# Performance work log

Hardware: AMD Instinct MI355X
Metric: run time of the kernel (lower is better)

Reference implementation:

```python
import jax, jax.numpy as jnp
import numpy as np

TEMPERATURE = 0.07
EPS = 1e-8  # torch cosine_similarity norm clamp


def setup_inputs() -> dict:
    key = jax.random.key(0)
    k1, k2 = jax.random.split(key)
    B, d = 8192, 256
    X = jax.random.normal(k1, (B, d), dtype=jnp.float32)
    Y = jax.random.normal(k2, (B, d), dtype=jnp.float32)
    return {"X": X, "Y": Y}


def _normalize(v):
    # torch cosine_similarity clamps the norm at eps
    n = jnp.sqrt(jnp.sum(v * v, axis=-1, keepdims=True))
    return v / jnp.maximum(n, EPS)


def reference(X, Y):
    # cosine similarity matrix via normalize + GEMM (same math as broadcasted
    # cosine_similarity(X.unsqueeze(1), Y.unsqueeze(0), dim=-1))
    Xn = _normalize(X)                      # [B, d]
    Yn = _normalize(Y)                      # [B, d]
    logits = (Xn @ Yn.T) / TEMPERATURE      # [B, B]
    # cross_entropy with targets = arange(B): mean of -log_softmax diagonal
    logp = jax.nn.log_softmax(logits, axis=-1)
    loss = -jnp.mean(jnp.diagonal(logp))
    return loss
```

## Files before the change

kernel.cpp:

```cpp
#include <hip/hip_runtime.h>
#include <hip/hip_bf16.h>


typedef __attribute__((ext_vector_type(2)))  float f32x2;
typedef __attribute__((ext_vector_type(4)))  float f32x4;
typedef __attribute__((ext_vector_type(4)))  int   i32x4;
typedef __attribute__((ext_vector_type(8)))  int   i32x8;

#define AS1(p) ((const __attribute__((address_space(1))) void*)(uintptr_t)(p))
#define AS3(p) ((__attribute__((address_space(3))) void*)(uintptr_t)(p))

constexpr int   BROWS = 8192;
constexpr int   DDIM  = 256;
constexpr float kInvT = 14.285714285714286f;
constexpr float kC1   = 20.609929155556622f;
constexpr float kLn2  = 0.6931471805599453f;
constexpr int   kSC   = 0x7F7F7F7F;

#if __has_builtin(__builtin_amdgcn_exp2f)
#define EXP2F(x) __builtin_amdgcn_exp2f(x)
#else
#define EXP2F(x) exp2f(x)
#endif
#if __has_builtin(__builtin_amdgcn_logf)
#define LOG2F(x) __builtin_amdgcn_logf(x)
#else
#define LOG2F(x) log2f(x)
#endif

static __device__ __forceinline__ unsigned f2fp8(float f) {
  unsigned u = __builtin_bit_cast(unsigned, f);
  unsigned s = (u >> 24) & 0x80u;
  float af = __builtin_fabsf(f);
  if (af < 0.015625f) {
    int q = (int)__builtin_rintf(af * 512.0f);
    return s | (unsigned)q;
  }
  unsigned au = u & 0x7FFFFFFFu;
  au += 0x7FFFFu + ((au >> 20) & 1u);
  unsigned e8 = ((au >> 23) - 127u + 7u) & 0xFu;
  unsigned m  = (au >> 20) & 7u;
  return s | (e8 << 3) | m;
}

__global__ __launch_bounds__(256) void nrm_kernel(
    const float* __restrict__ X, const float* __restrict__ Y,
    unsigned int* __restrict__ Xq, unsigned int* __restrict__ Yq,
    float* __restrict__ diag, float* __restrict__ row_sum)
{
  const int wave = threadIdx.x >> 6;
  const int lane = threadIdx.x & 63;
  const int row  = blockIdx.x * 4 + wave;
  const float4 x = *(const float4*)(X + (size_t)row * DDIM + lane * 4);
  const float4 y = *(const float4*)(Y + (size_t)row * DDIM + lane * 4);
  float ssx = x.x*x.x + x.y*x.y + x.z*x.z + x.w*x.w;
  float ssy = y.x*y.x + y.y*y.y + y.z*y.z + y.w*y.w;
  float dot = x.x*y.x + x.y*y.y + x.z*y.z + x.w*y.w;
  #pragma unroll
  for (int m = 1; m < 64; m <<= 1) {
    ssx += __shfl_xor(ssx, m);
    ssy += __shfl_xor(ssy, m);
    dot += __shfl_xor(dot, m);
  }
  const float invx = 1.0f / fmaxf(sqrtf(ssx), 1e-8f);
  const float invy = 1.0f / fmaxf(sqrtf(ssy), 1e-8f);
#if __has_builtin(__builtin_amdgcn_cvt_pk_fp8_f32)
  int xq = __builtin_amdgcn_cvt_pk_fp8_f32(x.x * invx, x.y * invx, 0, false);
  xq     = __builtin_amdgcn_cvt_pk_fp8_f32(x.z * invx, x.w * invx, xq, true);
  int yq = __builtin_amdgcn_cvt_pk_fp8_f32(y.x * invy, y.y * invy, 0, false);
  yq     = __builtin_amdgcn_cvt_pk_fp8_f32(y.z * invy, y.w * invy, yq, true);
#else
  int xq = (int)(f2fp8(x.x*invx) | (f2fp8(x.y*invx) << 8) |
                 (f2fp8(x.z*invx) << 16) | (f2fp8(x.w*invx) << 24));
  int yq = (int)(f2fp8(y.x*invy) | (f2fp8(y.y*invy) << 8) |
                 (f2fp8(y.z*invy) << 16) | (f2fp8(y.w*invy) << 24));
#endif
  Xq[row * 64 + lane] = (unsigned)xq;
  Yq[row * 64 + lane] = (unsigned)yq;
  if (lane == 0) {
    diag[row] = dot * invx * invy * kInvT;
    row_sum[row] = 0.0f;
  }
}

static __device__ __forceinline__ void expq(const f32x4& pv, f32x2 (&sm)[2]) {
  f32x2 v0 = { pv[0], pv[1] };
  f32x2 v1 = { pv[2], pv[3] };
  v0 = v0 * kC1 + (f32x2){-kC1, -kC1};
  v1 = v1 * kC1 + (f32x2){-kC1, -kC1};
  sm[0] += (f32x2){ EXP2F(v0.x), EXP2F(v0.y) };
  sm[1] += (f32x2){ EXP2F(v1.x), EXP2F(v1.y) };
}

static __device__ __forceinline__ void tile_step(
    const char* __restrict__ tb, const int (&bb)[2], const i32x8 (&a)[4][2],
    f32x4 (&cur)[4][2], f32x4 (&prev)[4][2], f32x2 (&sums2)[4][2])
{
  const f32x4 cz = {0.f, 0.f, 0.f, 0.f};
  {
    const i32x4 lo0 = *(const i32x4*)(tb + (bb[0]));
    const i32x4 hi0 = *(const i32x4*)(tb + (bb[0] ^ 16));
    const i32x4 lo1 = *(const i32x4*)(tb + (bb[1]));
    const i32x4 hi1 = *(const i32x4*)(tb + (bb[1] ^ 16));
    const i32x8 b0 = __builtin_shufflevector(lo0, hi0, 0, 1, 2, 3, 4, 5, 6, 7);
    const i32x8 b1 = __builtin_shufflevector(lo1, hi1, 0, 1, 2, 3, 4, 5, 6, 7);
    cur[0][0] = __builtin_amdgcn_mfma_scale_f32_16x16x128_f8f6f4(a[0][0], b0, cz, 0, 0, 0, kSC, 0, kSC);
    cur[0][1] = __builtin_amdgcn_mfma_scale_f32_16x16x128_f8f6f4(a[0][0], b1, cz, 0, 0, 0, kSC, 0, kSC);
    expq(prev[0][0], sums2[0]);
    cur[1][0] = __builtin_amdgcn_mfma_scale_f32_16x16x128_f8f6f4(a[1][0], b0, cz, 0, 0, 0, kSC, 0, kSC);
    cur[1][1] = __builtin_amdgcn_mfma_scale_f32_16x16x128_f8f6f4(a[1][0], b1, cz, 0, 0, 0, kSC, 0, kSC);
    expq(prev[1][0], sums2[1]);
    cur[2][0] = __builtin_amdgcn_mfma_scale_f32_16x16x128_f8f6f4(a[2][0], b0, cz, 0, 0, 0, kSC, 0, kSC);
    cur[2][1] = __builtin_amdgcn_mfma_scale_f32_16x16x128_f8f6f4(a[2][0], b1, cz, 0, 0, 0, kSC, 0, kSC);
    expq(prev[2][0], sums2[2]);
    cur[3][0] = __builtin_amdgcn_mfma_scale_f32_16x16x128_f8f6f4(a[3][0], b0, cz, 0, 0, 0, kSC, 0, kSC);
    cur[3][1] = __builtin_amdgcn_mfma_scale_f32_16x16x128_f8f6f4(a[3][0], b1, cz, 0, 0, 0, kSC, 0, kSC);
    expq(prev[3][0], sums2[3]);
  }
  {
    const i32x4 lo0 = *(const i32x4*)(tb + (bb[0] ^ 128));
    const i32x4 hi0 = *(const i32x4*)(tb + (bb[0] ^ 144));
    const i32x4 lo1 = *(const i32x4*)(tb + (bb[1] ^ 128));
    const i32x4 hi1 = *(const i32x4*)(tb + (bb[1] ^ 144));
    const i32x8 b0 = __builtin_shufflevector(lo0, hi0, 0, 1, 2, 3, 4, 5, 6, 7);
    const i32x8 b1 = __builtin_shufflevector(lo1, hi1, 0, 1, 2, 3, 4, 5, 6, 7);
    cur[0][0] = __builtin_amdgcn_mfma_scale_f32_16x16x128_f8f6f4(a[0][1], b0, cur[0][0], 0, 0, 0, kSC, 0, kSC);
    cur[0][1] = __builtin_amdgcn_mfma_scale_f32_16x16x128_f8f6f4(a[0][1], b1, cur[0][1], 0, 0, 0, kSC, 0, kSC);
    expq(prev[0][1], sums2[0]);
    cur[1][0] = __builtin_amdgcn_mfma_scale_f32_16x16x128_f8f6f4(a[1][1], b0, cur[1][0], 0, 0, 0, kSC, 0, kSC);
    cur[1][1] = __builtin_amdgcn_mfma_scale_f32_16x16x128_f8f6f4(a[1][1], b1, cur[1][1], 0, 0, 0, kSC, 0, kSC);
    expq(prev[1][1], sums2[1]);
    cur[2][0] = __builtin_amdgcn_mfma_scale_f32_16x16x128_f8f6f4(a[2][1], b0, cur[2][0], 0, 0, 0, kSC, 0, kSC);
    cur[2][1] = __builtin_amdgcn_mfma_scale_f32_16x16x128_f8f6f4(a[2][1], b1, cur[2][1], 0, 0, 0, kSC, 0, kSC);
    expq(prev[2][1], sums2[2]);
    cur[3][0] = __builtin_amdgcn_mfma_scale_f32_16x16x128_f8f6f4(a[3][1], b0, cur[3][0], 0, 0, 0, kSC, 0, kSC);
    cur[3][1] = __builtin_amdgcn_mfma_scale_f32_16x16x128_f8f6f4(a[3][1], b1, cur[3][1], 0, 0, 0, kSC, 0, kSC);
    expq(prev[3][1], sums2[3]);
  }
}

__global__ __launch_bounds__(256, 2) void logits_kernel(
    const unsigned char* __restrict__ Xq,
    const unsigned char* __restrict__ Yq,
    float* __restrict__ row_sum)
{
  __shared__ char lds[4 * 8192];
  const int tid  = threadIdx.x;
  const int lane = tid & 63;
  const int wave = tid >> 6;
  const int l15  = lane & 15;
  const int g    = lane >> 4;

  const int bid  = blockIdx.x;
  const int xcd  = bid & 7;
  const int idx  = bid >> 3;
  const int panel = (xcd >> 2) * 16 + (idx & 15);
  const int split = (xcd & 3) * 4 + (idx >> 4);

  const int rowbase = panel * 256 + wave * 64;
  const char* Xb = (const char*)Xq;
  const char* Yb = (const char*)Yq + (size_t)split * (512 * 256);

  i32x8 a[4][2];
  #pragma unroll
  for (int m = 0; m < 4; ++m) {
    const char* rp = Xb + (size_t)(rowbase + m * 16 + l15) * 256 + g * 32;
    a[m][0] = *(const i32x8*)(rp);
    a[m][1] = *(const i32x8*)(rp + 128);
  }

  f32x2 sums2[4][2];
  #pragma unroll
  for (int m = 0; m < 4; ++m) {
    sums2[m][0] = (f32x2){0.f, 0.f};
    sums2[m][1] = (f32x2){0.f, 0.f};
  }

  int bb[2];
  #pragma unroll
  for (int n = 0; n < 2; ++n)
    bb[n] = (n * 16 + l15) * 256 + (((2 * g) ^ l15) << 4);

  auto stage = [&](int t, int buf) {
    const char* Yt = Yb + (size_t)t * 8192;
    char* db = lds + buf * 8192;
    #pragma unroll
    for (int s = 0; s < 2; ++s) {
      const int portion = (s * 4 + wave) * 1024;
      const int L = portion + lane * 16;
      const int src = (L & ~255) | ((L & 255) ^ (((L >> 8) & 15) << 4));
      __builtin_amdgcn_global_load_lds(AS1(Yt + src), AS3(db + portion), 16, 0, 0);
    }
  };

  f32x4 accA[4][2], accB[4][2];
  #pragma unroll
  for (int m = 0; m < 4; ++m)
    #pragma unroll
    for (int n = 0; n < 2; ++n) {
      accA[m][n] = (f32x4){0.f, 0.f, 0.f, 0.f};
      const float ni = -__builtin_inff();
      accB[m][n] = (f32x4){ni, ni, ni, ni};
    }

  stage(0, 0);
  stage(1, 1);
  stage(2, 2);
  #pragma unroll 1
  for (int p = 0; p < 8; ++p) {
    const int t = 2 * p;
    if (p < 7) asm volatile("s_waitcnt vmcnt(4)" ::: "memory");
    else       asm volatile("s_waitcnt vmcnt(2)" ::: "memory");
    __builtin_amdgcn_s_barrier();
    if (t + 3 < 16) stage(t + 3, (t + 3) & 3);
    tile_step(lds + (t & 3) * 8192, bb, a, accA, accB, sums2);
    if (p < 7) asm volatile("s_waitcnt vmcnt(4)" ::: "memory");
    else       asm volatile("s_waitcnt vmcnt(0)" ::: "memory");
    __builtin_amdgcn_s_barrier();
    if (t + 4 < 16) stage(t + 4, (t + 4) & 3);
    tile_step(lds + ((t + 1) & 3) * 8192, bb, a, accB, accA, sums2);
  }
  #pragma unroll
  for (int m = 0; m < 4; ++m) {
    expq(accB[m][0], sums2[m]);
    expq(accB[m][1], sums2[m]);
  }

  #pragma unroll
  for (int m = 0; m < 4; ++m)
    #pragma unroll
    for (int h = 0; h < 2; ++h)
      #pragma unroll
      for (int r2 = 0; r2 < 2; ++r2) {
        float s = (r2 == 0) ? sums2[m][h].x : sums2[m][h].y;
        s += __shfl_xor(s, 1);
        s += __shfl_xor(s, 2);
        s += __shfl_xor(s, 4);
        s += __shfl_xor(s, 8);
        if (l15 == 0)
          atomicAdd(row_sum + rowbase + m * 16 + g * 4 + h * 2 + r2, s);
      }
}

__global__ __launch_bounds__(1024) void loss_kernel(
    const float* __restrict__ row_sum, const float* __restrict__ diag,
    float* __restrict__ out)
{
  const int t = threadIdx.x;
  double acc = 0.0;
  #pragma unroll
  for (int h = 0; h < 2; ++h) {
    const int i = h * 4096 + t * 4;
    const float4 s = *(const float4*)(row_sum + i);
    const float4 d = *(const float4*)(diag + i);
    acc += (double)(kInvT + LOG2F(s.x) * kLn2 - d.x);
    acc += (double)(kInvT + LOG2F(s.y) * kLn2 - d.y);
    acc += (double)(kInvT + LOG2F(s.z) * kLn2 - d.z);
    acc += (double)(kInvT + LOG2F(s.w) * kLn2 - d.w);
  }
  #pragma unroll
  for (int m = 1; m < 64; m <<= 1) acc += __shfl_xor(acc, m);
  __shared__ double red[16];
  if ((t & 63) == 0) red[t >> 6] = acc;
  __syncthreads();
  if (t == 0) {
    double tot = 0.0;
    #pragma unroll
    for (int w = 0; w < 16; ++w) tot += red[w];
    out[0] = (float)(tot / (double)BROWS);
  }
}

extern "C" void kernel_launch(void* const* d_in, const int* in_sizes, int n_in,
                              void* d_out, int out_size, void* d_ws, size_t ws_size,
                              hipStream_t stream) {
  (void)in_sizes; (void)n_in; (void)out_size; (void)ws_size;
  const float* X = (const float*)d_in[0];
  const float* Y = (const float*)d_in[1];
  char* w = (char*)d_ws;
  unsigned int* Xq = (unsigned int*)(w);
  unsigned int* Yq = (unsigned int*)(w + (2u << 20));
  float* diag    = (float*)(w + (4u << 20));
  float* row_sum = (float*)(w + (4u << 20) + (32u << 10));

  nrm_kernel<<<BROWS / 4, 256, 0, stream>>>(X, Y, Xq, Yq, diag, row_sum);
  logits_kernel<<<512, 256, 0, stream>>>((const unsigned char*)Xq,
                                         (const unsigned char*)Yq, row_sum);
  loss_kernel<<<1, 1024, 0, stream>>>(row_sum, diag, (float*)d_out);
}
```

Before: 35.43 us.

## Prefetch next tile's first-K B fragments from LDS into registers

Each tile step now loads the first-half B fragments of the following LDS tile into registers while it runs MFMAs on the current tile. The current tile's first-half fragments come from the previous step, and a prologue loads the first tile's fragments. The goal is to hide LDS read latency in front of the first MFMA group. In exchange, the global-to-LDS waits are tightened from vmcnt(4) to vmcnt(2) so the next tile is resident one step earlier, which leaves less slack for global load latency and adds register pressure.

Result: no change. 35.14 us (-0.8%).

```diff
diff --git a/kernel.cpp b/kernel.cpp
--- a/kernel.cpp
+++ b/kernel.cpp
@@ -27,6 +27,9 @@
 #else
 #define LOG2F(x) log2f(x)
 #endif
+
+#define MFMA __builtin_amdgcn_mfma_scale_f32_16x16x128_f8f6f4
+#define SHUF(lo, hi) __builtin_shufflevector(lo, hi, 0, 1, 2, 3, 4, 5, 6, 7)
 
 static __device__ __forceinline__ unsigned f2fp8(float f) {
   unsigned u = __builtin_bit_cast(unsigned, f);
@@ -92,51 +95,51 @@
   sm[1] += (f32x2){ EXP2F(v1.x), EXP2F(v1.y) };
 }
 
-static __device__ __forceinline__ void tile_step(
-    const char* __restrict__ tb, const int (&bb)[2], const i32x8 (&a)[4][2],
+static __device__ __forceinline__ void tile_compute(
+    const char* __restrict__ tb_cur, const char* __restrict__ tb_next,
+    bool doNext, const int (&bb)[2], const i32x8 (&a)[4][2],
+    i32x8 (&bK0)[2], i32x8 (&bN)[2],
     f32x4 (&cur)[4][2], f32x4 (&prev)[4][2], f32x2 (&sums2)[4][2])
 {
   const f32x4 cz = {0.f, 0.f, 0.f, 0.f};
-  {
-    const i32x4 lo0 = *(const i32x4*)(tb + (bb[0]));
-    const i32x4 hi0 = *(const i32x4*)(tb + (bb[0] ^ 16));
-    const i32x4 lo1 = *(const i32x4*)(tb + (bb[1]));
-    const i32x4 hi1 = *(const i32x4*)(tb + (bb[1] ^ 16));
-    const i32x8 b0 = __builtin_shufflevector(lo0, hi0, 0, 1, 2, 3, 4, 5, 6, 7);
-    const i32x8 b1 = __builtin_shufflevector(lo1, hi1, 0, 1, 2, 3, 4, 5, 6, 7);
-    cur[0][0] = __builtin_amdgcn_mfma_scale_f32_16x16x128_f8f6f4(a[0][0], b0, cz, 0, 0, 0, kSC, 0, kSC);
-    cur[0][1] = __builtin_amdgcn_mfma_scale_f32_16x16x128_f8f6f4(a[0][0], b1, cz, 0, 0, 0, kSC, 0, kSC);
-    expq(prev[0][0], sums2[0]);
-    cur[1][0] = __builtin_amdgcn_mfma_scale_f32_16x16x128_f8f6f4(a[1][0], b0, cz, 0, 0, 0, kSC, 0, kSC);
-    cur[1][1] = __builtin_amdgcn_mfma_scale_f32_16x16x128_f8f6f4(a[1][0], b1, cz, 0, 0, 0, kSC, 0, kSC);
-    expq(prev[1][0], sums2[1]);
-    cur[2][0] = __builtin_amdgcn_mfma_scale_f32_16x16x128_f8f6f4(a[2][0], b0, cz, 0, 0, 0, kSC, 0, kSC);
-    cur[2][1] = __builtin_amdgcn_mfma_scale_f32_16x16x128_f8f6f4(a[2][0], b1, cz, 0, 0, 0, kSC, 0, kSC);
-    expq(prev[2][0], sums2[2]);
-    cur[3][0] = __builtin_amdgcn_mfma_scale_f32_16x16x128_f8f6f4(a[3][0], b0, cz, 0, 0, 0, kSC, 0, kSC);
-    cur[3][1] = __builtin_amdgcn_mfma_scale_f32_16x16x128_f8f6f4(a[3][0], b1, cz, 0, 0, 0, kSC, 0, kSC);
-    expq(prev[3][0], sums2[3]);
-  }
-  {
-    const i32x4 lo0 = *(const i32x4*)(tb + (bb[0] ^ 128));
-    const i32x4 hi0 = *(const i32x4*)(tb + (bb[0] ^ 144));
-    const i32x4 lo1 = *(const i32x4*)(tb + (bb[1] ^ 128));
-    const i32x4 hi1 = *(const i32x4*)(tb + (bb[1] ^ 144));
-    const i32x8 b0 = __builtin_shufflevector(lo0, hi0, 0, 1, 2, 3, 4, 5, 6, 7);
-    const i32x8 b1 = __builtin_shufflevector(lo1, hi1, 0, 1, 2, 3, 4, 5, 6, 7);
-    cur[0][0] = __builtin_amdgcn_mfma_scale_f32_16x16x128_f8f6f4(a[0][1], b0, cur[0][0], 0, 0, 0, kSC, 0, kSC);
-    cur[0][1] = __builtin_amdgcn_mfma_scale_f32_16x16x128_f8f6f4(a[0][1], b1, cur[0][1], 0, 0, 0, kSC, 0, kSC);
-    expq(prev[0][1], sums2[0]);
-    cur[1][0] = __builtin_amdgcn_mfma_scale_f32_16x16x128_f8f6f4(a[1][1], b0, cur[1][0], 0, 0, 0, kSC, 0, kSC);
-    cur[1][1] = __builtin_amdgcn_mfma_scale_f32_16x16x128_f8f6f4(a[1][1], b1, cur[1][1], 0, 0, 0, kSC, 0, kSC);
-    expq(prev[1][1], sums2[1]);
-    cur[2][0] = __builtin_amdgcn_mfma_scale_f32_16x16x128_f8f6f4(a[2][1], b0, cur[2][0], 0, 0, 0, kSC, 0, kSC);
-    cur[2][1] = __builtin_amdgcn_mfma_scale_f32_16x16x128_f8f6f4(a[2][1], b1, cur[2][1], 0, 0, 0, kSC, 0, kSC);
-    expq(prev[2][1], sums2[2]);
-    cur[3][0] = __builtin_amdgcn_mfma_scale_f32_16x16x128_f8f6f4(a[3][1], b0, cur[3][0], 0, 0, 0, kSC, 0, kSC);
-    cur[3][1] = __builtin_amdgcn_mfma_scale_f32_16x16x128_f8f6f4(a[3][1], b1, cur[3][1], 0, 0, 0, kSC, 0, kSC);
-    expq(prev[3][1], sums2[3]);
-  }
+  const i32x4 lo0 = *(const i32x4*)(tb_cur + (bb[0] ^ 128));
+  const i32x4 hi0 = *(const i32x4*)(tb_cur + (bb[0] ^ 144));
+  const i32x4 lo1 = *(const i32x4*)(tb_cur + (bb[1] ^ 128));
+  const i32x4 hi1 = *(const i32x4*)(tb_cur + (bb[1] ^ 144));
+  if (doNext) {
+    const i32x4 nlo0 = *(const i32x4*)(tb_next + bb[0]);
+    const i32x4 nhi0 = *(const i32x4*)(tb_next + (bb[0] ^ 16));
+    const i32x4 nlo1 = *(const i32x4*)(tb_next + bb[1]);
+    const i32x4 nhi1 = *(const i32x4*)(tb_next + (bb[1] ^ 16));
+    bN[0] = SHUF(nlo0, nhi0);
+    bN[1] = SHUF(nlo1, nhi1);
+  }
+  cur[0][0] = MFMA(a[0][0], bK0[0], cz, 0, 0, 0, kSC, 0, kSC);
+  cur[0][1] = MFMA(a[0][0], bK0[1], cz, 0, 0, 0, kSC, 0, kSC);
+  expq(prev[0][0], sums2[0]);
+  cur[1][0] = MFMA(a[1][0], bK0[0], cz, 0, 0, 0, kSC, 0, kSC);
+  cur[1][1] = MFMA(a[1][0], bK0[1], cz, 0, 0, 0, kSC, 0, kSC);
+  expq(prev[1][0], sums2[1]);
+  cur[2][0] = MFMA(a[2][0], bK0[0], cz, 0, 0, 0, kSC, 0, kSC);
+  cur[2][1] = MFMA(a[2][0], bK0[1], cz, 0, 0, 0, kSC, 0, kSC);
+  expq(prev[2][0], sums2[2]);
+  cur[3][0] = MFMA(a[3][0], bK0[0], cz, 0, 0, 0, kSC, 0, kSC);
+  cur[3][1] = MFMA(a[3][0], bK0[1], cz, 0, 0, 0, kSC, 0, kSC);
+  expq(prev[3][0], sums2[3]);
+  const i32x8 b10 = SHUF(lo0, hi0);
+  const i32x8 b11 = SHUF(lo1, hi1);
+  cur[0][0] = MFMA(a[0][1], b10, cur[0][0], 0, 0, 0, kSC, 0, kSC);
+  cur[0][1] = MFMA(a[0][1], b11, cur[0][1], 0, 0, 0, kSC, 0, kSC);
+  expq(prev[0][1], sums2[0]);
+  cur[1][0] = MFMA(a[1][1], b10, cur[1][0], 0, 0, 0, kSC, 0, kSC);
+  cur[1][1] = MFMA(a[1][1], b11, cur[1][1], 0, 0, 0, kSC, 0, kSC);
+  expq(prev[1][1], sums2[1]);
+  cur[2][0] = MFMA(a[2][1], b10, cur[2][0], 0, 0, 0, kSC, 0, kSC);
+  cur[2][1] = MFMA(a[2][1], b11, cur[2][1], 0, 0, 0, kSC, 0, kSC);
+  expq(prev[2][1], sums2[2]);
+  cur[3][0] = MFMA(a[3][1], b10, cur[3][0], 0, 0, 0, kSC, 0, kSC);
+  cur[3][1] = MFMA(a[3][1], b11, cur[3][1], 0, 0, 0, kSC, 0, kSC);
+  expq(prev[3][1], sums2[3]);
 }
 
 __global__ __launch_bounds__(256, 2) void logits_kernel(
@@ -203,22 +206,37 @@
       accB[m][n] = (f32x4){ni, ni, ni, ni};
     }
 
+  i32x8 bA[2], bB[2];
+
   stage(0, 0);
   stage(1, 1);
   stage(2, 2);
+  asm volatile("s_waitcnt vmcnt(4)" ::: "memory");
+  __builtin_amdgcn_s_barrier();
+  {
+    const i32x4 plo0 = *(const i32x4*)(lds + bb[0]);
+    const i32x4 phi0 = *(const i32x4*)(lds + (bb[0] ^ 16));
+    const i32x4 plo1 = *(const i32x4*)(lds + bb[1]);
+    const i32x4 phi1 = *(const i32x4*)(lds + (bb[1] ^ 16));
+    bA[0] = SHUF(plo0, phi0);
+    bA[1] = SHUF(plo1, phi1);
+  }
+
   #pragma unroll 1
   for (int p = 0; p < 8; ++p) {
     const int t = 2 * p;
-    if (p < 7) asm volatile("s_waitcnt vmcnt(4)" ::: "memory");
-    else       asm volatile("s_waitcnt vmcnt(2)" ::: "memory");
+    if (p < 7) asm volatile("s_waitcnt vmcnt(2)" ::: "memory");
+    else       asm volatile("s_waitcnt vmcnt(0)" ::: "memory");
     __builtin_amdgcn_s_barrier();
     if (t + 3 < 16) stage(t + 3, (t + 3) & 3);
-    tile_step(lds + (t & 3) * 8192, bb, a, accA, accB, sums2);
-    if (p < 7) asm volatile("s_waitcnt vmcnt(4)" ::: "memory");
+    tile_compute(lds + (t & 3) * 8192, lds + ((t + 1) & 3) * 8192,
+                 true, bb, a, bA, bB, accA, accB, sums2);
+    if (p < 7) asm volatile("s_waitcnt vmcnt(2)" ::: "memory");
     else       asm volatile("s_waitcnt vmcnt(0)" ::: "memory");
     __builtin_amdgcn_s_barrier();
     if (t + 4 < 16) stage(t + 4, (t + 4) & 3);
-    tile_step(lds + ((t + 1) & 3) * 8192, bb, a, accB, accA, sums2);
+    tile_compute(lds + ((t + 1) & 3) * 8192, lds + ((t + 2) & 3) * 8192,
+                 (t + 2) < 16, bb, a, bB, bA, accB, accA, sums2);
   }
   #pragma unroll
   for (int m = 0; m < 4; ++m) {
```
